# Optimization experiments

Measured on AMD Instinct MI355X. Metric: run time of the kernel, lower is better.

## Reference

```python
import jax, jax.numpy as jnp
import numpy as np


def _lstm_cell(x, h, c, Wih, Whh, b):
    # PyTorch gate order: i, f, g, o
    g = x @ Wih.T + h @ Whh.T + b
    i, f, gg, o = jnp.split(g, 4, axis=-1)
    c2 = jax.nn.sigmoid(f) * c + jax.nn.sigmoid(i) * jnp.tanh(gg)
    h2 = jax.nn.sigmoid(o) * jnp.tanh(c2)
    return h2, c2


def _lstm_seq(x_tbd, h0, c0, Wih, Whh, b):
    # x_tbd: [T, B, D] -> outputs [T, B, H]
    def step(carry, xt):
        h, c = carry
        h2, c2 = _lstm_cell(xt, h, c, Wih, Whh, b)
        return (h2, c2), h2
    _, ys = jax.lax.scan(step, (h0, c0), x_tbd)
    return ys


def setup_inputs() -> dict:
    key = jax.random.key(0)
    ks = jax.random.split(key, 20)
    H, D, A, HOR, NQ = 256, 32, 128, 24, 3
    B, T = 256, 512
    s = 0.1
    inp = {
        'x':      jax.random.normal(ks[0], (B, T, D), jnp.float32),
        'e_Wih0': jax.random.normal(ks[1], (4 * H, D), jnp.float32) * s,
        'e_Whh0': jax.random.normal(ks[2], (4 * H, H), jnp.float32) * s,
        'e_b0':   jax.random.normal(ks[3], (4 * H,), jnp.float32) * s,
        'e_Wih1': jax.random.normal(ks[4], (4 * H, H), jnp.float32) * s,
        'e_Whh1': jax.random.normal(ks[5], (4 * H, H), jnp.float32) * s,
        'e_b1':   jax.random.normal(ks[6], (4 * H,), jnp.float32) * s,
        'd_Wih0': jax.random.normal(ks[7], (4 * H, 1), jnp.float32) * s,
        'd_Whh0': jax.random.normal(ks[8], (4 * H, H), jnp.float32) * s,
        'd_b0':   jax.random.normal(ks[9], (4 * H,), jnp.float32) * s,
        'd_Wih1': jax.random.normal(ks[10], (4 * H, H), jnp.float32) * s,
        'd_Whh1': jax.random.normal(ks[11], (4 * H, H), jnp.float32) * s,
        'd_b1':   jax.random.normal(ks[12], (4 * H,), jnp.float32) * s,
        'aW':     jax.random.normal(ks[13], (H, A), jnp.float32) * s,
        'aV':     jax.random.normal(ks[14], (A,), jnp.float32) * s,
        'qW':     jax.random.normal(ks[15], (NQ, HOR, H), jnp.float32) * s,
        'qb':     jax.random.normal(ks[16], (NQ, HOR), jnp.float32) * s,
    }
    return inp


def reference(x, e_Wih0, e_Whh0, e_b0, e_Wih1, e_Whh1, e_b1,
              d_Wih0, d_Whh0, d_b0, d_Wih1, d_Whh1, d_b1,
              aW, aV, qW, qb):
    B = x.shape[0]
    H = e_Whh0.shape[1]
    horizon = qW.shape[1]

    # ---- encoder: 2-layer LSTM over time ----
    xt = jnp.swapaxes(x, 0, 1)                      # [T, B, D]
    z = jnp.zeros((B, H), x.dtype)
    h1 = _lstm_seq(xt, z, z, e_Wih0, e_Whh0, e_b0)  # [T, B, H]
    h2 = _lstm_seq(h1, z, z, e_Wih1, e_Whh1, e_b1)  # [T, B, H]
    enc = jnp.swapaxes(h2, 0, 1)                    # [B, T, H]

    # ---- attention over encoder outputs ----
    energy = jnp.tanh(enc @ aW) @ aV                # [B, T]
    w = jax.nn.softmax(energy, axis=1)
    context = jnp.einsum('bt,bth->bh', w, enc)      # [B, H]

    inp0 = x[:, -1, -1:]                            # [B, 1]

    def dstep(carry, _):
        h0_, c0_, h1_, c1_, dinp = carry
        h0n, c0n = _lstm_cell(dinp, h0_, c0_, d_Wih0, d_Whh0, d_b0)
        h1n, c1n = _lstm_cell(h0n, h1_, c1_, d_Wih1, d_Whh1, d_b1)
        return (h0n, c0n, h1n, c1n, h1n[:, :1]), h1n

    _, douts = jax.lax.scan(dstep, (context, context, context, context, inp0),
                            None, length=horizon)   # [horizon, B, H]

    # ---- quantile heads on last decoder step ----
    last = douts[-1]                                # [B, H]
    preds = jnp.einsum('bh,qoh->bqo', last, qW) + qb  # [B, n_quantiles, horizon]
    return preds
```

## Files before the change

### kernel.cpp

```cpp
#include <hip/hip_runtime.h>

typedef unsigned short u16;
typedef unsigned int u32;
typedef unsigned long long u64;
typedef short v8s __attribute__((ext_vector_type(8)));
typedef float v4f __attribute__((ext_vector_type(4)));


__device__ __forceinline__ float bf2f(u16 u) { union { u32 u; float f; } c; c.u = ((u32)u) << 16; return c.f; }
__device__ __forceinline__ u16 f2bf(float f) {
  union { float f; u32 u; } c; c.f = f;
  u32 r = c.u + 0x7FFFu + ((c.u >> 16) & 1u);
  return (u16)(r >> 16);
}
__device__ __forceinline__ float sigf(float x) { return 1.f / (1.f + __expf(-x)); }
__device__ __forceinline__ float tanhfast(float x) {
  x = fminf(15.f, fmaxf(-15.f, x));
  float e = __expf(2.f * x);
  return (e - 1.f) / (e + 1.f);
}
__device__ __forceinline__ float ldIn(const void* p, size_t i, int isbf) {
  return isbf ? bf2f(((const u16*)p)[i]) : ((const float*)p)[i];
}
__device__ __forceinline__ v8s ld8hi(const void* p, size_t e, int isbf) {
  if (isbf) return *(const v8s*)((const u16*)p + e);
  const float* f = (const float*)p + e;
  v8s r;
#pragma unroll
  for (int j = 0; j < 8; ++j) r[j] = (short)f2bf(f[j]);
  return r;
}
__device__ __forceinline__ void ld8split(const void* p, size_t e, int isbf, v8s& hi, v8s& lo) {
  if (isbf) {
    hi = *(const v8s*)((const u16*)p + e);
    lo = v8s{0, 0, 0, 0, 0, 0, 0, 0};
  } else {
    const float* f = (const float*)p + e;
#pragma unroll
    for (int j = 0; j < 8; ++j) {
      u16 h = f2bf(f[j]);
      hi[j] = (short)h;
      lo[j] = (short)f2bf(f[j] - bf2f(h));
    }
  }
}
#define MFMA(a, b, c) __builtin_amdgcn_mfma_f32_16x16x32_bf16(a, b, c, 0, 0, 0)

__device__ __forceinline__ u64 aload64(const u64* p) {
  return __hip_atomic_load(p, __ATOMIC_RELAXED, __HIP_MEMORY_SCOPE_AGENT);
}
__device__ __forceinline__ void astore32(u32* p, u32 v) {
  __hip_atomic_store(p, v, __ATOMIC_RELAXED, __HIP_MEMORY_SCOPE_AGENT);
}
__device__ __forceinline__ void astore64(u64* p, u64 v) {
  __hip_atomic_store(p, v, __ATOMIC_RELAXED, __HIP_MEMORY_SCOPE_AGENT);
}

__device__ __forceinline__ void stage_enc(u16* h0s, u16* h1s,
                                          const u32* s0, const u32* s1,
                                          int tid, u32 tag, bool doH0) {
  const u64* p0 = (const u64*)s0;
  const u64* p1 = (const u64*)s1;
  u64 v0[8], v1[8];
#pragma unroll
  for (int i = 0; i < 8; ++i) {
    if (doH0) v0[i] = aload64(p0 + i * 256 + tid);
    v1[i] = aload64(p1 + i * 256 + tid);
  }
  bool all;
  do {
    all = true;
#pragma unroll
    for (int i = 0; i < 8; ++i) {
      if (doH0) {
        u64 w = v0[i];
        if (!((((w >> 16) & 0xFFFFull) == tag) && ((w >> 48) == tag))) {
          all = false;
          v0[i] = aload64(p0 + i * 256 + tid);
        }
      }
      u64 w1 = v1[i];
      if (!((((w1 >> 16) & 0xFFFFull) == tag) && ((w1 >> 48) == tag))) {
        all = false;
        v1[i] = aload64(p1 + i * 256 + tid);
      }
    }
  } while (!all);
#pragma unroll
  for (int i = 0; i < 8; ++i) {
    int idx = i * 256 + tid;
    int row = idx >> 7, jp = idx & 127;
    if (doH0) {
      u64 w = v0[i];
      ((u32*)(h0s + row * 264))[jp] = (u32)(w & 0xFFFF) | (((u32)(w >> 32) & 0xFFFF) << 16);
    }
    u64 w = v1[i];
    ((u32*)(h1s + row * 264))[jp] = (u32)(w & 0xFFFF) | (((u32)(w >> 32) & 0xFFFF) << 16);
  }
}

__device__ __forceinline__ void stage_dec(u16* dhi, u16* dlo, const u64* src,
                                          int tid, u32 tag) {
  u64 v[16];
#pragma unroll
  for (int i = 0; i < 16; ++i) v[i] = aload64(src + i * 256 + tid);
  bool all;
  do {
    all = true;
#pragma unroll
    for (int i = 0; i < 16; ++i) {
      if ((u32)(v[i] >> 32) != tag) { all = false; v[i] = aload64(src + i * 256 + tid); }
    }
  } while (!all);
#pragma unroll
  for (int i = 0; i < 16; ++i) {
    int idx = i * 256 + tid;
    int row = idx >> 8, col = idx & 255;
    dhi[row * 264 + col] = (u16)v[i];
    dlo[row * 264 + col] = (u16)(v[i] >> 16);
  }
}
__device__ __forceinline__ void stage_f32(u16* dhi, u16* dlo, const float* src, int tid) {
#pragma unroll
  for (int i = 0; i < 8; ++i) {
    int e = i * 512 + tid * 2;
    int row = e >> 8, jc = e & 255;
    float f0 = src[row * 256 + jc], f1 = src[row * 256 + jc + 1];
    u16 h0 = f2bf(f0), h1 = f2bf(f1);
    u16 l0 = f2bf(f0 - bf2f(h0)), l1 = f2bf(f1 - bf2f(h1));
    ((u32*)(dhi + row * 264))[jc >> 1] = (u32)h0 | ((u32)h1 << 16);
    ((u32*)(dlo + row * 264))[jc >> 1] = (u32)l0 | ((u32)l1 << 16);
  }
}

__global__ void sniff_kernel(const u16* __restrict__ w, int* __restrict__ flag) {
  __shared__ int cnt;
  if (threadIdx.x == 0) cnt = 0;
  __syncthreads();
  int ok = 0;
  for (int i = threadIdx.x; i < 1024; i += 256) {
    u16 u = w[2 * i];
    int e = (u >> 7) & 0xFF;
    ok += (u == 0 || (e >= 97 && e <= 140)) ? 1 : 0;
  }
  atomicAdd(&cnt, ok);
  __syncthreads();
  if (threadIdx.x == 0) *flag = (cnt >= 768) ? 1 : 0;
}

__global__ __launch_bounds__(256, 1) void enc_kernel(
    const void* __restrict__ x,
    const void* __restrict__ eWih0, const void* __restrict__ eWhh0, const void* __restrict__ eb0,
    const void* __restrict__ eWih1, const void* __restrict__ eWhh1, const void* __restrict__ eb1,
    const void* __restrict__ aW, const void* __restrict__ aV,
    u32* __restrict__ H0, u32* __restrict__ H1,
    float* __restrict__ ctx, const int* __restrict__ flagp) {
  __shared__ u16 h0s[16 * 264], h1s[16 * 264];
  __shared__ float gb0[16 * 64], gb1[16 * 64];
  __shared__ float eP[16 * 132];

  const int isbf = *flagp;
  const int tid = threadIdx.x, blk = blockIdx.x;
  const int grp = blk & 15, gs = blk >> 4;
  const int lane = tid & 63, wv = tid >> 6;
  const int ln = lane & 15, lq = lane >> 4;

  v8s W0F[9], W1F[16], AWF[16];
  {
    const int gw = wv * 256 + gs * 16 + ln;
    const int kq = lq * 8;
    W0F[0] = ld8hi(eWih0, (size_t)gw * 32 + kq, isbf);
#pragma unroll
    for (int kt = 0; kt < 8; ++kt) {
      W0F[kt + 1] = ld8hi(eWhh0, (size_t)gw * 256 + kt * 32 + kq, isbf);
      W1F[kt]     = ld8hi(eWhh1, (size_t)gw * 256 + kt * 32 + kq, isbf);
      W1F[kt + 8] = ld8hi(eWih1, (size_t)gw * 256 + kt * 32 + kq, isbf);
    }
#pragma unroll
    for (int kt = 0; kt < 8; ++kt)
#pragma unroll
      for (int j2 = 0; j2 < 2; ++j2) {
        v8s f;
        int ac = (2 * wv + j2) * 16 + ln;
#pragma unroll
        for (int j = 0; j < 8; ++j)
          f[j] = (short)f2bf(ldIn(aW, (size_t)(kt * 32 + kq + j) * 128 + ac, isbf));
        AWF[kt * 2 + j2] = f;
      }
  }

  const int urow = tid >> 4, uu = tid & 15;
  float bg0[4], bg1[4], aVr[8];
#pragma unroll
  for (int g = 0; g < 4; ++g) {
    bg0[g] = ldIn(eb0, g * 256 + gs * 16 + uu, isbf);
    bg1[g] = ldIn(eb1, g * 256 + gs * 16 + uu, isbf);
  }
#pragma unroll
  for (int j = 0; j < 8; ++j) aVr[j] = ldIn(aV, (size_t)(uu + 16 * j), isbf);

  const int gRowU = grp * 16 + urow;
  const int gUnit = gs * 16 + uu;
  const int aRow = grp * 16 + ln;

  float c0 = 0.f, c1 = 0.f;
  float mS = -3e38f, lS = 0.f, ctxA = 0.f;

  v8s xh_c, xl_c;
  ld8split(x, ((size_t)aRow * 512) * 32 + lq * 8, isbf, xh_c, xl_c);

#pragma unroll 1
  for (int t = 0; t < 514; ++t) {
    const int rB = (t + 1) & 1, wB = t & 1;
    stage_enc(h0s, h1s,
              H0 + (size_t)rB * 65536 + grp * 4096,
              H1 + (size_t)wB * 65536 + grp * 4096,
              tid, (u32)(u16)t, t <= 512);
    v8s xh_n, xl_n;
    {
      int tn = (t + 1 < 512) ? t + 1 : 511;
      ld8split(x, ((size_t)aRow * 512 + tn) * 32 + lq * 8, isbf, xh_n, xl_n);
    }
    __syncthreads();

    v4f acc0 = {0, 0, 0, 0}, acc1 = {0, 0, 0, 0}, accA0 = {0, 0, 0, 0}, accA1 = {0, 0, 0, 0};
    acc0 = MFMA(xh_c, W0F[0], acc0);
    if (!isbf) acc0 = MFMA(xl_c, W0F[0], acc0);
#pragma unroll
    for (int kt = 0; kt < 8; ++kt) {
      const int off = ln * 264 + kt * 32 + lq * 8;
      v8s a0 = *(const v8s*)(h0s + off);
      acc0 = MFMA(a0, W0F[kt + 1], acc0);
      acc1 = MFMA(a0, W1F[kt + 8], acc1);
      v8s a1 = *(const v8s*)(h1s + off);
      acc1 = MFMA(a1, W1F[kt], acc1);
      accA0 = MFMA(a1, AWF[kt * 2], accA0);
      accA1 = MFMA(a1, AWF[kt * 2 + 1], accA1);
    }
    {
      const int bR = lq * 4;
#pragma unroll
      for (int r = 0; r < 4; ++r) {
        gb0[(bR + r) * 64 + ln * 4 + wv] = acc0[r];
        gb1[(bR + r) * 64 + ln * 4 + wv] = acc1[r];
        eP[(bR + r) * 132 + (2 * wv) * 16 + ln] = accA0[r];
        eP[(bR + r) * 132 + (2 * wv + 1) * 16 + ln] = accA1[r];
      }
    }
    float h1v = bf2f(h1s[urow * 264 + gUnit]);
    __syncthreads();

    const u32 tagS = (u32)(u16)(t + 1) << 16;
    if (t < 512) {
      const float* g0 = gb0 + (urow * 16 + uu) * 4;
      float gi = g0[0] + bg0[0], gf = g0[1] + bg0[1], gg = g0[2] + bg0[2], go = g0[3] + bg0[3];
      c0 = sigf(gf) * c0 + sigf(gi) * tanhfast(gg);
      float h = sigf(go) * tanhfast(c0);
      astore32(H0 + (size_t)wB * 65536 + gRowU * 256 + gUnit, (u32)f2bf(h) | tagS);
    }
    if (t >= 1 && t < 513) {
      const float* g1 = gb1 + (urow * 16 + uu) * 4;
      float gi = g1[0] + bg1[0], gf = g1[1] + bg1[1], gg = g1[2] + bg1[2], go = g1[3] + bg1[3];
      c1 = sigf(gf) * c1 + sigf(gi) * tanhfast(gg);
      float h = sigf(go) * tanhfast(c1);
      astore32(H1 + (size_t)rB * 65536 + gRowU * 256 + gUnit, (u32)f2bf(h) | tagS);
    } else if (t == 0) {
      astore32(H1 + (size_t)rB * 65536 + gRowU * 256 + gUnit, tagS);
    }
    if (t >= 2) {
      float e = 0.f;
#pragma unroll
      for (int j = 0; j < 8; ++j)
        e += tanhfast(eP[urow * 132 + uu + 16 * j]) * aVr[j];
      e += __shfl_xor(e, 1);
      e += __shfl_xor(e, 2);
      e += __shfl_xor(e, 4);
      e += __shfl_xor(e, 8);
      float nm = fmaxf(mS, e);
      float al = __expf(mS - nm), p = __expf(e - nm);
      lS = lS * al + p;
      ctxA = ctxA * al + p * h1v;
      mS = nm;
    }
    xh_c = xh_n; xl_c = xl_n;
  }
  ctx[(size_t)gRowU * 256 + gUnit] = ctxA / lS;
}

__global__ __launch_bounds__(256, 1) void dec_kernel(
    const void* __restrict__ x,
    const void* __restrict__ dWih0, const void* __restrict__ dWhh0, const void* __restrict__ db0,
    const void* __restrict__ dWih1, const void* __restrict__ dWhh1, const void* __restrict__ db1,
    const void* __restrict__ qW, const void* __restrict__ qb,
    const float* __restrict__ ctx,
    u64* __restrict__ H0d, u64* __restrict__ H1d, u64* __restrict__ dinpG,
    void* __restrict__ out, const int* __restrict__ flagp) {
  __shared__ u16 sAhi[16 * 264], sAlo[16 * 264], sBhi[16 * 264], sBlo[16 * 264];
  __shared__ float gb[16 * 64];
  __shared__ float dinpS[16];

  const int isbf = *flagp;
  const int tid = threadIdx.x, blk = blockIdx.x;
  const int grp = blk & 15, gs = blk >> 4;
  const int lane = tid & 63, wv = tid >> 6;
  const int ln = lane & 15, lq = lane >> 4;

  v8s W0F[8], W1F[16];
  {
    const int gw = wv * 256 + gs * 16 + ln;
    const int kq = lq * 8;
#pragma unroll
    for (int kt = 0; kt < 8; ++kt) {
      W0F[kt]     = ld8hi(dWhh0, (size_t)gw * 256 + kt * 32 + kq, isbf);
      W1F[kt]     = ld8hi(dWhh1, (size_t)gw * 256 + kt * 32 + kq, isbf);
      W1F[kt + 8] = ld8hi(dWih1, (size_t)gw * 256 + kt * 32 + kq, isbf);
    }
  }
  const int urow = tid >> 4, uu = tid & 15;
  float bg0[4], bg1[4], w0v[4];
#pragma unroll
  for (int g = 0; g < 4; ++g) {
    bg0[g] = ldIn(db0, g * 256 + gs * 16 + uu, isbf);
    bg1[g] = ldIn(db1, g * 256 + gs * 16 + uu, isbf);
    w0v[g] = ldIn(dWih0, g * 256 + gs * 16 + uu, isbf);
  }
  const int gRowU = grp * 16 + urow;
  const int gUnit = gs * 16 + uu;

  float c0 = ctx[(size_t)gRowU * 256 + gUnit];
  float c1 = c0;

#pragma unroll 1
  for (int t = 0; t < 24; ++t) {
    const int pPrev = (t + 1) & 1, pCur = t & 1;
    if (t == 0) {
      stage_f32(sAhi, sAlo, ctx + (size_t)grp * 16 * 256, tid);
      if (tid < 16)
        dinpS[tid] = ldIn(x, ((size_t)(grp * 16 + tid) * 512 + 511) * 32 + 31, isbf);
    } else {
      stage_dec(sAhi, sAlo, H0d + (size_t)pPrev * 65536 + grp * 4096, tid, (u32)(2 * t - 1));
      if (tid < 16) {
        u64 w;
        do { w = aload64(dinpG + pPrev * 256 + grp * 16 + tid); } while ((u32)(w >> 32) != (u32)(2 * t));
        dinpS[tid] = __uint_as_float((u32)w);
      }
    }
    __syncthreads();
    v4f acc = {0, 0, 0, 0};
#pragma unroll
    for (int kt = 0; kt < 8; ++kt) {
      const int off = ln * 264 + kt * 32 + lq * 8;
      acc = MFMA(*(const v8s*)(sAhi + off), W0F[kt], acc);
      acc = MFMA(*(const v8s*)(sAlo + off), W0F[kt], acc);
    }
    {
      const int bR = lq * 4;
#pragma unroll
      for (int r = 0; r < 4; ++r) gb[(bR + r) * 64 + ln * 4 + wv] = acc[r];
    }
    float di = dinpS[urow];
    __syncthreads();
    {
      const float* g0 = gb + (urow * 16 + uu) * 4;
      float gi = g0[0] + bg0[0] + di * w0v[0];
      float gf = g0[1] + bg0[1] + di * w0v[1];
      float gg = g0[2] + bg0[2] + di * w0v[2];
      float go = g0[3] + bg0[3] + di * w0v[3];
      c0 = sigf(gf) * c0 + sigf(gi) * tanhfast(gg);
      float h = sigf(go) * tanhfast(c0);
      u16 hh = f2bf(h); u16 hl = f2bf(h - bf2f(hh));
      astore64(H0d + (size_t)pCur * 65536 + gRowU * 256 + gUnit,
               (u64)hh | ((u64)hl << 16) | ((u64)(u32)(2 * t + 1) << 32));
    }
    if (t == 0) stage_f32(sBhi, sBlo, ctx + (size_t)grp * 16 * 256, tid);
    else stage_dec(sBhi, sBlo, H1d + (size_t)pPrev * 65536 + grp * 4096, tid, (u32)(2 * t));
    stage_dec(sAhi, sAlo, H0d + (size_t)pCur * 65536 + grp * 4096, tid, (u32)(2 * t + 1));
    __syncthreads();
    v4f a1 = {0, 0, 0, 0};
#pragma unroll
    for (int kt = 0; kt < 8; ++kt) {
      const int off = ln * 264 + kt * 32 + lq * 8;
      a1 = MFMA(*(const v8s*)(sBhi + off), W1F[kt], a1);
      a1 = MFMA(*(const v8s*)(sBlo + off), W1F[kt], a1);
      a1 = MFMA(*(const v8s*)(sAhi + off), W1F[kt + 8], a1);
      a1 = MFMA(*(const v8s*)(sAlo + off), W1F[kt + 8], a1);
    }
    {
      const int bR = lq * 4;
#pragma unroll
      for (int r = 0; r < 4; ++r) gb[(bR + r) * 64 + ln * 4 + wv] = a1[r];
    }
    __syncthreads();
    {
      const float* g1 = gb + (urow * 16 + uu) * 4;
      float gi = g1[0] + bg1[0], gf = g1[1] + bg1[1], gg = g1[2] + bg1[2], go = g1[3] + bg1[3];
      c1 = sigf(gf) * c1 + sigf(gi) * tanhfast(gg);
      float h = sigf(go) * tanhfast(c1);
      u16 hh = f2bf(h); u16 hl = f2bf(h - bf2f(hh));
      astore64(H1d + (size_t)pCur * 65536 + gRowU * 256 + gUnit,
               (u64)hh | ((u64)hl << 16) | ((u64)(u32)(2 * t + 2) << 32));
      if (gUnit == 0)
        astore64(dinpG + pCur * 256 + gRowU,
                 (u64)__float_as_uint(h) | ((u64)(u32)(2 * t + 2) << 32));
    }
  }
  stage_dec(sAhi, sAlo, H1d + (size_t)65536 + grp * 4096, tid, 48u);
  __syncthreads();
  if (gs < 12 && tid < 96) {
    int r = tid / 6, p = tid % 6;
    int qo = gs * 6 + p, row = grp * 16 + r;
    float s = ldIn(qb, qo, isbf);
    for (int h = 0; h < 256; ++h)
      s += (bf2f(sAhi[r * 264 + h]) + bf2f(sAlo[r * 264 + h])) * ldIn(qW, (size_t)qo * 256 + h, isbf);
    if (isbf) ((u16*)out)[row * 72 + qo] = f2bf(s);
    else      ((float*)out)[row * 72 + qo] = s;
  }
}

extern "C" void kernel_launch(void* const* d_in, const int* in_sizes, int n_in,
                              void* d_out, int out_size, void* d_ws, size_t ws_size,
                              hipStream_t stream) {
  const void* x     = d_in[0];
  const void* eWih0 = d_in[1];
  const void* eWhh0 = d_in[2];
  const void* eb0   = d_in[3];
  const void* eWih1 = d_in[4];
  const void* eWhh1 = d_in[5];
  const void* eb1   = d_in[6];
  const void* dWih0 = d_in[7];
  const void* dWhh0 = d_in[8];
  const void* db0   = d_in[9];
  const void* dWih1 = d_in[10];
  const void* dWhh1 = d_in[11];
  const void* db1   = d_in[12];
  const void* aW    = d_in[13];
  const void* aV    = d_in[14];
  const void* qW    = d_in[15];
  const void* qb    = d_in[16];

  char* wsb = (char*)d_ws;
  u32*   H0    = (u32*)(wsb + 0);
  u32*   H1    = (u32*)(wsb + 524288);
  int*   flag  = (int*)(wsb + 1048576);
  float* ctx   = (float*)(wsb + 1048832);
  u64*   dinpG = (u64*)(wsb + 1310976);
  u64*   H0d   = (u64*)(wsb + 1315072);
  u64*   H1d   = (u64*)(wsb + 2363648);

  hipMemsetAsync(wsb, 0, 1048576, stream);

  sniff_kernel<<<1, 256, 0, stream>>>((const u16*)eWhh0, flag);
  enc_kernel<<<256, 256, 0, stream>>>(x, eWih0, eWhh0, eb0, eWih1, eWhh1, eb1,
                                      aW, aV, H0, H1, ctx, flag);
  dec_kernel<<<256, 256, 0, stream>>>(x, dWih0, dWhh0, db0, dWih1, dWhh1, db1,
                                      qW, qb, ctx, H0d, H1d, dinpG,
                                      d_out, flag);
}
```

Baseline: 2.304 ms.

## Split encoder step into layer-0 and layer-1 phases with early H0 publish

The combined per-step staging of both layers' hidden states is split. Layer 0 now stages H0, computes its gates and publishes the new H0 before waiting on H1, so the dependent layer-0 chain across blocks is no longer gated on layer-1 arrival. The next H0 poll is issued early to overlap its latency. The global H buffer layout and shared-memory tiles are also changed, with XOR swizzling and padded gate buffers, to cut LDS bank conflicts. This adds an extra __syncthreads per step and more live registers (a0r, v0s, v1s).

```diff
diff --git a/kernel.cpp b/kernel.cpp
--- a/kernel.cpp
+++ b/kernel.cpp
@@ -56,46 +56,33 @@
   __hip_atomic_store(p, v, __ATOMIC_RELAXED, __HIP_MEMORY_SCOPE_AGENT);
 }
 
-__device__ __forceinline__ void stage_enc(u16* h0s, u16* h1s,
-                                          const u32* s0, const u32* s1,
-                                          int tid, u32 tag, bool doH0) {
-  const u64* p0 = (const u64*)s0;
-  const u64* p1 = (const u64*)s1;
-  u64 v0[8], v1[8];
-#pragma unroll
-  for (int i = 0; i < 8; ++i) {
-    if (doH0) v0[i] = aload64(p0 + i * 256 + tid);
-    v1[i] = aload64(p1 + i * 256 + tid);
-  }
+__device__ __forceinline__ void stage_issue(u64* v, const u32* src, int tid) {
+  const u64* p = (const u64*)src;
+#pragma unroll
+  for (int i = 0; i < 8; ++i) v[i] = aload64(p + i * 256 + tid);
+}
+__device__ __forceinline__ void stage_finish(u16* dst, const u32* src, u64* v, int tid, u32 tag) {
+  const u64* p = (const u64*)src;
   bool all;
   do {
     all = true;
 #pragma unroll
     for (int i = 0; i < 8; ++i) {
-      if (doH0) {
-        u64 w = v0[i];
-        if (!((((w >> 16) & 0xFFFFull) == tag) && ((w >> 48) == tag))) {
-          all = false;
-          v0[i] = aload64(p0 + i * 256 + tid);
-        }
-      }
-      u64 w1 = v1[i];
-      if (!((((w1 >> 16) & 0xFFFFull) == tag) && ((w1 >> 48) == tag))) {
+      u64 w = v[i];
+      if (!((((w >> 16) & 0xFFFFull) == tag) && ((w >> 48) == tag))) {
         all = false;
-        v1[i] = aload64(p1 + i * 256 + tid);
+        v[i] = aload64(p + i * 256 + tid);
       }
     }
   } while (!all);
 #pragma unroll
   for (int i = 0; i < 8; ++i) {
     int idx = i * 256 + tid;
-    int row = idx >> 7, jp = idx & 127;
-    if (doH0) {
-      u64 w = v0[i];
-      ((u32*)(h0s + row * 264))[jp] = (u32)(w & 0xFFFF) | (((u32)(w >> 32) & 0xFFFF) << 16);
-    }
-    u64 w = v1[i];
-    ((u32*)(h1s + row * 264))[jp] = (u32)(w & 0xFFFF) | (((u32)(w >> 32) & 0xFFFF) << 16);
+    int row = (idx >> 3) & 15;
+    int jp  = ((idx >> 7) << 3) | (idx & 7);
+    u64 w = v[i];
+    u32 val = (u32)(w & 0xFFFF) | ((((u32)(w >> 32)) & 0xFFFF) << 16);
+    *(u32*)(dst + row * 264 + ((jp * 2) ^ ((row & 7) << 3))) = val;
   }
 }
 
@@ -155,8 +142,8 @@
     const void* __restrict__ aW, const void* __restrict__ aV,
     u32* __restrict__ H0, u32* __restrict__ H1,
     float* __restrict__ ctx, const int* __restrict__ flagp) {
-  __shared__ u16 h0s[16 * 264], h1s[16 * 264];
-  __shared__ float gb0[16 * 64], gb1[16 * 64];
+  __shared__ __align__(16) u16 h0s[16 * 264], h1s[16 * 264];
+  __shared__ float gb0[16 * 66], gb1[16 * 66];
   __shared__ float eP[16 * 132];
 
   const int isbf = *flagp;
@@ -202,20 +189,72 @@
   const int gRowU = grp * 16 + urow;
   const int gUnit = gs * 16 + uu;
   const int aRow = grp * 16 + ln;
+  const u32 stOff = (u32)(grp * 4096 + gs * 256 + urow * 16 + uu);
 
   float c0 = 0.f, c1 = 0.f;
   float mS = -3e38f, lS = 0.f, ctxA = 0.f;
 
   v8s xh_c, xl_c;
   ld8split(x, ((size_t)aRow * 512) * 32 + lq * 8, isbf, xh_c, xl_c);
+
+  u64 v0s[8];
+  stage_issue(v0s, H0 + (size_t)1 * 65536 + grp * 4096, tid);
+  v8s a0r[8];
 
 #pragma unroll 1
   for (int t = 0; t < 514; ++t) {
     const int rB = (t + 1) & 1, wB = t & 1;
-    stage_enc(h0s, h1s,
-              H0 + (size_t)rB * 65536 + grp * 4096,
-              H1 + (size_t)wB * 65536 + grp * 4096,
-              tid, (u32)(u16)t, t <= 512);
+    const u32 tag = (u32)(u16)t;
+    if (t <= 512)
+      stage_finish(h0s, H0 + (size_t)rB * 65536 + grp * 4096, v0s, tid, tag);
+    __syncthreads();
+
+    if (t <= 512) {
+#pragma unroll
+      for (int kt = 0; kt < 8; ++kt)
+        a0r[kt] = *(const v8s*)(h0s + ln * 264 + ((kt * 32 + lq * 8) ^ ((ln & 7) << 3)));
+    }
+    if (t < 512) {
+      v4f acc0 = {0, 0, 0, 0};
+      acc0 = MFMA(xh_c, W0F[0], acc0);
+      if (!isbf) acc0 = MFMA(xl_c, W0F[0], acc0);
+#pragma unroll
+      for (int kt = 0; kt < 8; ++kt) acc0 = MFMA(a0r[kt], W0F[kt + 1], acc0);
+#pragma unroll
+      for (int r = 0; r < 4; ++r) gb0[(lq * 4 + r) * 66 + wv * 16 + ln] = acc0[r];
+    }
+    __syncthreads();
+
+    u64 v1s[8];
+    stage_issue(v1s, H1 + (size_t)wB * 65536 + grp * 4096, tid);
+    const u32 tagS = (u32)(u16)(t + 1) << 16;
+    if (t < 512) {
+      float gi = gb0[urow * 66 + uu]      + bg0[0];
+      float gf = gb0[urow * 66 + 16 + uu] + bg0[1];
+      float gg = gb0[urow * 66 + 32 + uu] + bg0[2];
+      float go = gb0[urow * 66 + 48 + uu] + bg0[3];
+      c0 = sigf(gf) * c0 + sigf(gi) * tanhfast(gg);
+      float h = sigf(go) * tanhfast(c0);
+      astore32(H0 + (size_t)wB * 65536 + stOff, (u32)f2bf(h) | tagS);
+    }
+    stage_finish(h1s, H1 + (size_t)wB * 65536 + grp * 4096, v1s, tid, tag);
+    __syncthreads();
+
+    v4f acc1 = {0, 0, 0, 0}, accA0 = {0, 0, 0, 0}, accA1 = {0, 0, 0, 0};
+#pragma unroll
+    for (int kt = 0; kt < 8; ++kt) {
+      v8s a1 = *(const v8s*)(h1s + ln * 264 + ((kt * 32 + lq * 8) ^ ((ln & 7) << 3)));
+      acc1 = MFMA(a0r[kt], W1F[kt + 8], acc1);
+      acc1 = MFMA(a1, W1F[kt], acc1);
+      accA0 = MFMA(a1, AWF[kt * 2], accA0);
+      accA1 = MFMA(a1, AWF[kt * 2 + 1], accA1);
+    }
+#pragma unroll
+    for (int r = 0; r < 4; ++r) {
+      gb1[(lq * 4 + r) * 66 + wv * 16 + ln] = acc1[r];
+      eP[(lq * 4 + r) * 132 + (2 * wv) * 16 + ln] = accA0[r];
+      eP[(lq * 4 + r) * 132 + (2 * wv + 1) * 16 + ln] = accA1[r];
+    }
     v8s xh_n, xl_n;
     {
       int tn = (t + 1 < 512) ? t + 1 : 511;
@@ -223,51 +262,21 @@
     }
     __syncthreads();
 
-    v4f acc0 = {0, 0, 0, 0}, acc1 = {0, 0, 0, 0}, accA0 = {0, 0, 0, 0}, accA1 = {0, 0, 0, 0};
-    acc0 = MFMA(xh_c, W0F[0], acc0);
-    if (!isbf) acc0 = MFMA(xl_c, W0F[0], acc0);
-#pragma unroll
-    for (int kt = 0; kt < 8; ++kt) {
-      const int off = ln * 264 + kt * 32 + lq * 8;
-      v8s a0 = *(const v8s*)(h0s + off);
-      acc0 = MFMA(a0, W0F[kt + 1], acc0);
-      acc1 = MFMA(a0, W1F[kt + 8], acc1);
-      v8s a1 = *(const v8s*)(h1s + off);
-      acc1 = MFMA(a1, W1F[kt], acc1);
-      accA0 = MFMA(a1, AWF[kt * 2], accA0);
-      accA1 = MFMA(a1, AWF[kt * 2 + 1], accA1);
-    }
-    {
-      const int bR = lq * 4;
-#pragma unroll
-      for (int r = 0; r < 4; ++r) {
-        gb0[(bR + r) * 64 + ln * 4 + wv] = acc0[r];
-        gb1[(bR + r) * 64 + ln * 4 + wv] = acc1[r];
-        eP[(bR + r) * 132 + (2 * wv) * 16 + ln] = accA0[r];
-        eP[(bR + r) * 132 + (2 * wv + 1) * 16 + ln] = accA1[r];
-      }
-    }
-    float h1v = bf2f(h1s[urow * 264 + gUnit]);
-    __syncthreads();
-
-    const u32 tagS = (u32)(u16)(t + 1) << 16;
-    if (t < 512) {
-      const float* g0 = gb0 + (urow * 16 + uu) * 4;
-      float gi = g0[0] + bg0[0], gf = g0[1] + bg0[1], gg = g0[2] + bg0[2], go = g0[3] + bg0[3];
-      c0 = sigf(gf) * c0 + sigf(gi) * tanhfast(gg);
-      float h = sigf(go) * tanhfast(c0);
-      astore32(H0 + (size_t)wB * 65536 + gRowU * 256 + gUnit, (u32)f2bf(h) | tagS);
-    }
     if (t >= 1 && t < 513) {
-      const float* g1 = gb1 + (urow * 16 + uu) * 4;
-      float gi = g1[0] + bg1[0], gf = g1[1] + bg1[1], gg = g1[2] + bg1[2], go = g1[3] + bg1[3];
+      float gi = gb1[urow * 66 + uu]      + bg1[0];
+      float gf = gb1[urow * 66 + 16 + uu] + bg1[1];
+      float gg = gb1[urow * 66 + 32 + uu] + bg1[2];
+      float go = gb1[urow * 66 + 48 + uu] + bg1[3];
       c1 = sigf(gf) * c1 + sigf(gi) * tanhfast(gg);
       float h = sigf(go) * tanhfast(c1);
-      astore32(H1 + (size_t)rB * 65536 + gRowU * 256 + gUnit, (u32)f2bf(h) | tagS);
+      astore32(H1 + (size_t)rB * 65536 + stOff, (u32)f2bf(h) | tagS);
     } else if (t == 0) {
-      astore32(H1 + (size_t)rB * 65536 + gRowU * 256 + gUnit, tagS);
-    }
+      astore32(H1 + (size_t)rB * 65536 + stOff, tagS);
+    }
+    if (t + 1 <= 512)
+      stage_issue(v0s, H0 + (size_t)((t + 2) & 1) * 65536 + grp * 4096, tid);
     if (t >= 2) {
+      float h1v = bf2f(h1s[urow * 264 + (gUnit ^ ((urow & 7) << 3))]);
       float e = 0.f;
 #pragma unroll
       for (int j = 0; j < 8; ++j)
```

Result: no change. 2.270 ms (-1.5%).
